# Kernel tuning notes

Measured on AMD Instinct MI355X. Metric: run time of the kernel, lower is better.

Reference implementation:

```python
import jax, jax.numpy as jnp
import numpy as np


def decode_e4m3(bits):
    """Decode raw FP8 E4M3 byte patterns (int32 in [0,256)) to float32.

    Layout: 1 sign bit, 4 exponent bits (bias 7), 3 mantissa bits.
    exp==0 -> subnormal: mant/8 * 2^-6. The NaN pattern (exp==15, man==7)
    is remapped to the max normal magnitude 448 to keep the reference
    NaN-free for randomized inputs.
    """
    b = bits.astype(jnp.int32)
    sign = jnp.where((b & 0x80) != 0, -1.0, 1.0).astype(jnp.float32)
    exp = (b >> 3) & 0xF
    man = (b & 0x7).astype(jnp.float32)
    # remap NaN encoding (exp=15, man=7) to max normal 448 = (1+6/8)*2^8
    man = jnp.where((exp == 15) & (man == 7.0), 6.0, man)
    sub = man * jnp.float32(2.0 ** -9)                     # man/8 * 2^-6
    norm = (1.0 + man / 8.0) * jnp.exp2((exp - 7).astype(jnp.float32))
    return sign * jnp.where(exp == 0, sub, norm)


def setup_inputs() -> dict:
    key = jax.random.key(0)
    k1, k2, k3, k4 = jax.random.split(key, 4)
    T, D_IN, D_OUT = 8192, 4096, 8192  # tokens (2x4096), in_features, out_features
    x = jax.random.normal(k1, (T, D_IN), dtype=jnp.float32)
    weight_fp8 = jax.random.randint(k2, (D_OUT, D_IN), 0, 256, dtype=jnp.int32)
    weight_scales = jax.random.uniform(k3, (D_OUT,), dtype=jnp.float32)
    bias = jax.random.normal(k4, (D_OUT,), dtype=jnp.float32)
    return {"x": x, "weight_fp8": weight_fp8, "weight_scales": weight_scales, "bias": bias}


def reference(x, weight_fp8, weight_scales, bias):
    # Fused FP8 dequant + GEMM + bias: W = decode(w_fp8) * scale[:, None]
    w = decode_e4m3(weight_fp8) * weight_scales[:, None]   # [out, in]
    return jnp.einsum("ti,oi->to", x, w) + bias[None, :]
```

## Files before the change

### kernel.cpp

```cpp
#include <hip/hip_runtime.h>

using short8 = __attribute__((ext_vector_type(8))) short;
using bf16x8 = __attribute__((ext_vector_type(8))) __bf16;
using f32x4  = __attribute__((ext_vector_type(4))) float;

__device__ __forceinline__ void gload_lds16(const void* g, void* l) {
  __builtin_amdgcn_global_load_lds(
      (const __attribute__((address_space(1))) void*)g,
      (__attribute__((address_space(3))) void*)l, 16, 0, 0);
}


__device__ __forceinline__ float dec_e4m3(int b) {
  int e = (b >> 3) & 15;
  int m = b & 7;
  if (e == 15 && m == 7) m = 6;
  float v;
  if (e) v = (1.0f + (float)m * 0.125f) * __uint_as_float((unsigned)(e + 120) << 23);
  else   v = (float)m * 0.001953125f;
  return (b & 0x80) ? -v : v;
}

__global__ void dec_w_kernel(const int* __restrict__ wq,
                             unsigned short* __restrict__ wb, int n8) {
  int i = blockIdx.x * blockDim.x + threadIdx.x;
  if (i >= n8) return;
  const int4* p = (const int4*)wq + (size_t)i * 2;
  int4 a = p[0], b4 = p[1];
  int bv[8] = {a.x, a.y, a.z, a.w, b4.x, b4.y, b4.z, b4.w};
  short8 r;
#pragma unroll
  for (int j = 0; j < 8; ++j) {
    float f = dec_e4m3(bv[j]);
    r[j] = (short)(__float_as_uint(f) >> 16);
  }
  *(short8*)(wb + (size_t)i * 8) = r;
}

__global__ void cvt_x_kernel(const float* __restrict__ x,
                             unsigned short* __restrict__ xb, int n8) {
  int i = blockIdx.x * blockDim.x + threadIdx.x;
  if (i >= n8) return;
  const float4* p = (const float4*)x + (size_t)i * 2;
  float4 a = p[0], b4 = p[1];
  float v[8] = {a.x, a.y, a.z, a.w, b4.x, b4.y, b4.z, b4.w};
  short8 r;
#pragma unroll
  for (int j = 0; j < 8; ++j) {
    unsigned u = __float_as_uint(v[j]);
    u += 0x7FFFu + ((u >> 16) & 1u);
    r[j] = (short)(u >> 16);
  }
  *(short8*)(xb + (size_t)i * 8) = r;
}


#define NOPV ((void)0)
#define VM6 asm volatile("s_waitcnt vmcnt(6)" ::: "memory")
#define VM0 asm volatile("s_waitcnt vmcnt(0)" ::: "memory")

#define STAGE_A(GP, LBUF, KT, J) do { \
    const char* _g = (GP) + (size_t)(KT) * 128u; \
    gload_lds16(_g + (size_t)((J) * 64) * Kb, (LBUF) + ((J) * 64) * 128 + tdA); \
    gload_lds16(_g + (size_t)(128 + (J) * 64) * Kb, (LBUF) + (128 + (J) * 64) * 128 + tdA); \
  } while (0)

#define STAGE_B(GP, LBUF, KT, J) do { \
    const char* _g = (GP) + (size_t)(KT) * 128u; \
    gload_lds16(_g + (size_t)((J) * 32) * Kb, (LBUF) + ((J) * 32) * 128 + tdB); \
    gload_lds16(_g + (size_t)(128 + (J) * 32) * Kb, (LBUF) + (128 + (J) * 32) * 128 + tdB); \
  } while (0)

#define PHASE(QM, QN, DOA, DOB, STAGE, LGK8, VM) { \
    if (DOA) { \
      _Pragma("unroll") \
      for (int mi = 0; mi < 4; ++mi) { \
        const char* _b = lA + (size_t)(arow + (QM) * 64 + mi * 16) * 128; \
        a[mi][0] = *(const bf16x8*)(_b + fo0); \
        a[mi][1] = *(const bf16x8*)(_b + fo1); \
      } \
    } \
    if (DOB) { \
      _Pragma("unroll") \
      for (int ni = 0; ni < 2; ++ni) { \
        const char* _b = lB + (size_t)(brow + ((QN) * 2 + ni) * 16) * 128; \
        b[(QN) * 2 + ni][0] = *(const bf16x8*)(_b + fo0); \
        b[(QN) * 2 + ni][1] = *(const bf16x8*)(_b + fo1); \
      } \
    } \
    STAGE; \
    if (LGK8) asm volatile("s_waitcnt lgkmcnt(8)" ::: "memory"); \
    __builtin_amdgcn_s_barrier(); \
    asm volatile("s_waitcnt lgkmcnt(0)" ::: "memory"); \
    __builtin_amdgcn_sched_barrier(0); \
    __builtin_amdgcn_s_setprio(1); \
    _Pragma("unroll") \
    for (int mi = 0; mi < 4; ++mi) \
      _Pragma("unroll") \
      for (int ni = 0; ni < 2; ++ni) \
        _Pragma("unroll") \
        for (int ks = 0; ks < 2; ++ks) \
          acc[(QM) * 4 + mi][(QN) * 2 + ni] = __builtin_amdgcn_mfma_f32_16x16x32_bf16( \
              a[mi][ks], b[(QN) * 2 + ni][ks], acc[(QM) * 4 + mi][(QN) * 2 + ni], 0, 0, 0); \
    __builtin_amdgcn_s_setprio(0); \
    VM; \
    __builtin_amdgcn_s_barrier(); \
  }

__global__ __launch_bounds__(512, 2) void gemm256_kernel(
    const unsigned short* __restrict__ A, const unsigned short* __restrict__ B,
    const float* __restrict__ scale, const float* __restrict__ bias,
    float* __restrict__ out, int T, int K, int N) {
  extern __shared__ char lds[];
  char* const lA0 = lds;
  char* const lB0 = lds + 32768;
  char* const lA1 = lds + 65536;
  char* const lB1 = lds + 98304;

  const int nbn = N >> 8;
  const int nbm = T >> 8;
  int bm, bn, CH;
  if (((nbm & 3) == 0) && ((nbn & 7) == 0) &&
      (int)gridDim.x == (nbm >> 2) * nbn) {
    const int xcd = blockIdx.x & 7, off = blockIdx.x >> 3;
    const int cpx = nbn >> 3;
    const int col = xcd * cpx + (off % cpx);
    const int ci  = off / cpx;
    bm = (ci * 4) << 8;
    bn = col << 8;
    CH = 4;
  } else {
    const int nwg = nbm * nbn;
    const int q = nwg >> 3, r = nwg & 7;
    const int xcd = blockIdx.x & 7, off = blockIdx.x >> 3;
    const int swz = (xcd < r ? xcd * (q + 1) : r * (q + 1) + (xcd - r) * q) + off;
    bm = (swz / nbn) << 8;
    bn = (swz % nbn) << 8;
    CH = 1;
  }

  const int tid = threadIdx.x;
  const int wave = tid >> 6, lane = tid & 63;
  const int wm = wave >> 2, wn = wave & 3;
  const int nt = K >> 6;
  const size_t Kb = (size_t)K * 2;

  const int trow = tid >> 3;
  const int gcol = ((tid & 7) * 16) ^ (((tid >> 3) & 7) << 4);
  const int bmap = ((tid & 256) ? 64 : 0) + ((tid >> 6) & 3) * 8 + ((tid >> 3) & 7);
  const char* gAb = (const char*)A + (size_t)(bm + trow) * Kb + gcol;
  const char* gBb = (const char*)B + (size_t)(bn + bmap) * Kb + gcol;
  const int tdA = tid * 16;
  const int tdB = bmap * 128 + (tid & 7) * 16;

  const int g16 = lane >> 4, l8 = lane & 7;
  const int fo0 = ((g16 ^ l8) << 4);
  const int fo1 = fo0 ^ 64;
  const int arow = wm * 128 + (lane & 15);
  const int brow = wn * 64 + (lane & 15);

  const int ccol = bn + wn * 64 + (lane & 15);
  int crow = bm + wm * 128 + ((lane >> 4) << 2);
  float scv[4], biv[4];
#pragma unroll
  for (int ni = 0; ni < 4; ++ni) {
    scv[ni] = scale[ccol + ni * 16];
    biv[ni] = bias[ccol + ni * 16];
  }

  f32x4 acc[8][4] = {};
  bf16x8 a[4][2], b[4][2];
  const char *lA, *lB;

  for (int ch = 0; ch < CH; ++ch) {
    const bool more = (ch + 1 < CH);
    const char* gAn = gAb + (size_t)256 * Kb;

    if (ch == 0) {
      STAGE_A(gAb, lA0, 0, 0);
      STAGE_B(gBb, lB0, 0, 0);
      STAGE_B(gBb, lB0, 0, 1);
      STAGE_A(gAb, lA0, 0, 1);
      STAGE_A(gAb, lA1, 1, 0);
      STAGE_B(gBb, lB1, 1, 0);
      STAGE_B(gBb, lB1, 1, 1);
      VM6;
      __builtin_amdgcn_s_barrier();
    }

    int t = 0;
    for (; t + 3 < nt; t += 2) {
      lA = lA0; lB = lB0;
      PHASE(0, 0, 1, 1, STAGE_A(gAb, lA1, t + 1, 1), 1, NOPV)
      PHASE(0, 1, 0, 1, STAGE_A(gAb, lA0, t + 2, 0), 0, NOPV)
      PHASE(1, 1, 1, 0, STAGE_B(gBb, lB0, t + 2, 0), 0, NOPV)
      PHASE(1, 0, 0, 0, STAGE_B(gBb, lB0, t + 2, 1), 0, VM6)
      lA = lA1; lB = lB1;
      PHASE(0, 0, 1, 1, STAGE_A(gAb, lA0, t + 2, 1), 1, NOPV)
      PHASE(0, 1, 0, 1, STAGE_A(gAb, lA1, t + 3, 0), 0, NOPV)
      PHASE(1, 1, 1, 0, STAGE_B(gBb, lB1, t + 3, 0), 0, NOPV)
      PHASE(1, 0, 0, 0, STAGE_B(gBb, lB1, t + 3, 1), 0, VM6)
    }
    lA = lA0; lB = lB0;
    PHASE(0, 0, 1, 1, STAGE_A(gAb, lA1, t + 1, 1), 1, NOPV)
    PHASE(0, 1, 0, 1, NOPV, 0, NOPV)
    PHASE(1, 1, 1, 0, NOPV, 0, NOPV)
    PHASE(1, 0, 0, 0, NOPV, 0, VM0)
    lA = lA1; lB = lB1;
    PHASE(0, 0, 1, 1, { if (more) STAGE_A(gAn, lA0, 0, 0); }, 1, NOPV)
    PHASE(0, 1, 0, 1, { if (more) STAGE_B(gBb, lB0, 0, 0); }, 0, NOPV)
    PHASE(1, 1, 1, 0, { if (more) STAGE_B(gBb, lB0, 0, 1); }, 0, NOPV)
    PHASE(1, 0, 0, 0, { if (more) STAGE_A(gAn, lA0, 0, 1); }, 0, NOPV)

#pragma unroll
    for (int ni = 0; ni < 4; ++ni) {
      const int o = ccol + ni * 16;
#pragma unroll
      for (int mi = 0; mi < 8; ++mi) {
#pragma unroll
        for (int rr = 0; rr < 4; ++rr) {
          __builtin_nontemporal_store(acc[mi][ni][rr] * scv[ni] + biv[ni],
                                      &out[(size_t)(crow + mi * 16 + rr) * N + o]);
        }
      }
    }

    if (more) {
#pragma unroll
      for (int mi = 0; mi < 8; ++mi)
#pragma unroll
        for (int ni = 0; ni < 4; ++ni)
          acc[mi][ni] = (f32x4){0.f, 0.f, 0.f, 0.f};
      STAGE_A(gAn, lA1, 1, 0);
      STAGE_B(gBb, lB1, 1, 0);
      STAGE_B(gBb, lB1, 1, 1);
      VM6;
      __builtin_amdgcn_s_barrier();
      gAb = gAn;
      crow += 256;
    }
  }
}


#define BM 128
#define BN 128
#define BK 64

__global__ __launch_bounds__(256) void gemm_bf16_kernel(
    const unsigned short* __restrict__ A, const unsigned short* __restrict__ B,
    const float* __restrict__ scale, const float* __restrict__ bias,
    float* __restrict__ out, int T, int K, int N) {
  __shared__ __align__(16) unsigned short lsA[BM * BK];
  __shared__ __align__(16) unsigned short lsB[BN * BK];

  const int nbn = N / BN;
  const int nwg = (T / BM) * nbn;
  const int q = nwg >> 3, r = nwg & 7;
  const int xcd = blockIdx.x & 7, off = blockIdx.x >> 3;
  const int swz = (xcd < r ? xcd * (q + 1) : r * (q + 1) + (xcd - r) * q) + off;
  const int bm = (swz / nbn) * BM;
  const int bn = (swz % nbn) * BN;

  const int tid = threadIdx.x;
  const int wave = tid >> 6, lane = tid & 63;
  const int wm = (wave >> 1) * 64, wn = (wave & 1) * 64;

  f32x4 acc[4][4] = {};

  const int srow = (wave << 3) + (lane >> 3);
  const int scolb = (lane & 7) * 16;
  const size_t Kb = (size_t)K * 2;
  const char* gA = (const char*)A + (size_t)bm * Kb + scolb;
  const char* gB = (const char*)B + (size_t)bn * Kb + scolb;
  char* laddrA = (char*)lsA + wave * 1024;
  char* laddrB = (char*)lsB + wave * 1024;

  for (int k0 = 0; k0 < K; k0 += BK) {
    const char* pa = gA + (size_t)k0 * 2;
    const char* pb = gB + (size_t)k0 * 2;
#pragma unroll
    for (int s = 0; s < 4; ++s) {
      int row = s * 32 + srow;
      gload_lds16(pa + (size_t)row * Kb, laddrA + s * 4096);
      gload_lds16(pb + (size_t)row * Kb, laddrB + s * 4096);
    }
    __syncthreads();

    const int arow2 = wm + (lane & 15);
    const int brow2 = wn + (lane & 15);
#pragma unroll
    for (int kk = 0; kk < BK; kk += 32) {
      const int kcol = kk + ((lane >> 4) << 3);
      bf16x8 af[4], bfr[4];
#pragma unroll
      for (int i = 0; i < 4; ++i)
        af[i] = *(const bf16x8*)(lsA + (size_t)(arow2 + i * 16) * BK + kcol);
#pragma unroll
      for (int i = 0; i < 4; ++i)
        bfr[i] = *(const bf16x8*)(lsB + (size_t)(brow2 + i * 16) * BK + kcol);
#pragma unroll
      for (int mi = 0; mi < 4; ++mi)
#pragma unroll
        for (int ni = 0; ni < 4; ++ni)
          acc[mi][ni] = __builtin_amdgcn_mfma_f32_16x16x32_bf16(
              af[mi], bfr[ni], acc[mi][ni], 0, 0, 0);
    }
    __syncthreads();
  }

  const int ccol = bn + wn + (lane & 15);
  const int crow0 = bm + wm + ((lane >> 4) << 2);
#pragma unroll
  for (int ni = 0; ni < 4; ++ni) {
    const int o = ccol + ni * 16;
    const float sc = scale[o], bi = bias[o];
#pragma unroll
    for (int mi = 0; mi < 4; ++mi) {
#pragma unroll
      for (int rr = 0; rr < 4; ++rr) {
        const int t2 = crow0 + mi * 16 + rr;
        out[(size_t)t2 * N + o] = acc[mi][ni][rr] * sc + bi;
      }
    }
  }
}


__global__ void naive_kernel(const float* __restrict__ X, const int* __restrict__ Wq,
                             const float* __restrict__ sc, const float* __restrict__ bs,
                             float* __restrict__ out, int T, int K, int N) {
  __shared__ float xt[16][16];
  __shared__ float wt[16][17];
  const int tx = threadIdx.x & 15, ty = threadIdx.x >> 4;
  const int t = blockIdx.y * 16 + ty, o = blockIdx.x * 16 + tx;
  float acc = 0.f;
  for (int k0 = 0; k0 < K; k0 += 16) {
    xt[ty][tx] = X[(size_t)t * K + k0 + tx];
    wt[ty][tx] = dec_e4m3(Wq[(size_t)(blockIdx.x * 16 + ty) * K + k0 + tx]);
    __syncthreads();
#pragma unroll
    for (int kk = 0; kk < 16; ++kk) acc += xt[ty][kk] * wt[tx][kk];
    __syncthreads();
  }
  out[(size_t)t * N + o] = acc * sc[o] + bs[o];
}

extern "C" void kernel_launch(void* const* d_in, const int* in_sizes, int n_in,
                              void* d_out, int out_size, void* d_ws, size_t ws_size,
                              hipStream_t stream) {
  const float* x  = (const float*)d_in[0];
  const int*   wq = (const int*)d_in[1];
  const float* sc = (const float*)d_in[2];
  const float* bi = (const float*)d_in[3];
  float* out = (float*)d_out;

  const int DOUT = in_sizes[2];
  const int DIN  = in_sizes[1] / DOUT;
  const int T    = in_sizes[0] / DIN;

  const size_t need = ((size_t)T * DIN + (size_t)DOUT * DIN) * 2;
  const bool ok256 = (T % 256 == 0) && (DOUT % 256 == 0) && (DIN % 256 == 0);
  const bool ok128 = (T % BM == 0) && (DOUT % BN == 0) && (DIN % BK == 0);

  if (ws_size >= need && (ok256 || ok128)) {
    unsigned short* xb = (unsigned short*)d_ws;
    unsigned short* wb = xb + (size_t)T * DIN;
    const int nx8 = (int)((size_t)T * DIN / 8);
    const int nw8 = (int)((size_t)DOUT * DIN / 8);
    cvt_x_kernel<<<(nx8 + 255) / 256, 256, 0, stream>>>(x, xb, nx8);
    dec_w_kernel<<<(nw8 + 255) / 256, 256, 0, stream>>>(wq, wb, nw8);
    if (ok256) {
      const int nbm = T >> 8, nbn = DOUT >> 8;
      const bool okchain = ((nbm & 3) == 0) && ((nbn & 7) == 0);
      const int grid = okchain ? (nbm >> 2) * nbn : nbm * nbn;
      gemm256_kernel<<<grid, 512, 131072, stream>>>(xb, wb, sc, bi, out, T, DIN, DOUT);
    } else {
      dim3 grid((T / BM) * (DOUT / BN));
      gemm_bf16_kernel<<<grid, 256, 0, stream>>>(xb, wb, sc, bi, out, T, DIN, DOUT);
    }
  } else {
    dim3 g(DOUT / 16, T / 16);
    naive_kernel<<<g, 256, 0, stream>>>(x, wq, sc, bi, out, T, DIN, DOUT);
  }
}
```

Baseline: 515.2 us.

## Software-pipeline LDS fragment reads one phase ahead of MFMA compute

```diff
diff --git a/kernel.cpp b/kernel.cpp
--- a/kernel.cpp
+++ b/kernel.cpp
@@ -71,26 +71,25 @@
     gload_lds16(_g + (size_t)(128 + (J) * 32) * Kb, (LBUF) + (128 + (J) * 32) * 128 + tdB); \
   } while (0)
 
-#define PHASE(QM, QN, DOA, DOB, STAGE, LGK8, VM) { \
-    if (DOA) { \
-      _Pragma("unroll") \
-      for (int mi = 0; mi < 4; ++mi) { \
-        const char* _b = lA + (size_t)(arow + (QM) * 64 + mi * 16) * 128; \
-        a[mi][0] = *(const bf16x8*)(_b + fo0); \
-        a[mi][1] = *(const bf16x8*)(_b + fo1); \
-      } \
+#define RD_A(DST, LB, QM) do { \
+    _Pragma("unroll") \
+    for (int mi = 0; mi < 4; ++mi) { \
+      const char* _b = lds + (LB) + (size_t)(arow + (QM) * 64 + mi * 16) * 128; \
+      (DST)[mi * 2 + 0] = *(const bf16x8*)(_b + fo0); \
+      (DST)[mi * 2 + 1] = *(const bf16x8*)(_b + fo1); \
     } \
-    if (DOB) { \
-      _Pragma("unroll") \
-      for (int ni = 0; ni < 2; ++ni) { \
-        const char* _b = lB + (size_t)(brow + ((QN) * 2 + ni) * 16) * 128; \
-        b[(QN) * 2 + ni][0] = *(const bf16x8*)(_b + fo0); \
-        b[(QN) * 2 + ni][1] = *(const bf16x8*)(_b + fo1); \
-      } \
+  } while (0)
+
+#define RD_B(DST, LB, QN) do { \
+    _Pragma("unroll") \
+    for (int ni = 0; ni < 2; ++ni) { \
+      const char* _b = lds + (LB) + (size_t)(brow + ((QN) * 2 + ni) * 16) * 128; \
+      (DST)[ni * 2 + 0] = *(const bf16x8*)(_b + fo0); \
+      (DST)[ni * 2 + 1] = *(const bf16x8*)(_b + fo1); \
     } \
-    STAGE; \
-    if (LGK8) asm volatile("s_waitcnt lgkmcnt(8)" ::: "memory"); \
-    __builtin_amdgcn_s_barrier(); \
+  } while (0)
+
+#define PH(AB, BB, QM, QN, STBLK, VMBLK, PFBLK) do { \
     asm volatile("s_waitcnt lgkmcnt(0)" ::: "memory"); \
     __builtin_amdgcn_sched_barrier(0); \
     __builtin_amdgcn_s_setprio(1); \
@@ -101,11 +100,13 @@
         _Pragma("unroll") \
         for (int ks = 0; ks < 2; ++ks) \
           acc[(QM) * 4 + mi][(QN) * 2 + ni] = __builtin_amdgcn_mfma_f32_16x16x32_bf16( \
-              a[mi][ks], b[(QN) * 2 + ni][ks], acc[(QM) * 4 + mi][(QN) * 2 + ni], 0, 0, 0); \
+              (AB)[mi * 2 + ks], (BB)[ni * 2 + ks], acc[(QM) * 4 + mi][(QN) * 2 + ni], 0, 0, 0); \
     __builtin_amdgcn_s_setprio(0); \
-    VM; \
+    STBLK; \
+    VMBLK; \
+    PFBLK; \
     __builtin_amdgcn_s_barrier(); \
-  }
+  } while (0)
 
 __global__ __launch_bounds__(512, 2) void gemm256_kernel(
     const unsigned short* __restrict__ A, const unsigned short* __restrict__ B,
@@ -116,6 +117,7 @@
   char* const lB0 = lds + 32768;
   char* const lA1 = lds + 65536;
   char* const lB1 = lds + 98304;
+  const int L0A = 0, L0B = 32768, L1A = 65536, L1B = 98304;
 
   const int nbn = N >> 8;
   const int nbm = T >> 8;
@@ -169,8 +171,7 @@
   }
 
   f32x4 acc[8][4] = {};
-  bf16x8 a[4][2], b[4][2];
-  const char *lA, *lB;
+  bf16x8 aE[8], aO[8], b0a[4], b0b[4], b1[4];
 
   for (int ch = 0; ch < CH; ++ch) {
     const bool more = (ch + 1 < CH);
@@ -186,31 +187,31 @@
       STAGE_B(gBb, lB1, 1, 1);
       VM6;
       __builtin_amdgcn_s_barrier();
+      RD_A(aE, L0A, 0);
+      RD_B(b0a, L0B, 0);
     }
 
     int t = 0;
     for (; t + 3 < nt; t += 2) {
-      lA = lA0; lB = lB0;
-      PHASE(0, 0, 1, 1, STAGE_A(gAb, lA1, t + 1, 1), 1, NOPV)
-      PHASE(0, 1, 0, 1, STAGE_A(gAb, lA0, t + 2, 0), 0, NOPV)
-      PHASE(1, 1, 1, 0, STAGE_B(gBb, lB0, t + 2, 0), 0, NOPV)
-      PHASE(1, 0, 0, 0, STAGE_B(gBb, lB0, t + 2, 1), 0, VM6)
-      lA = lA1; lB = lB1;
-      PHASE(0, 0, 1, 1, STAGE_A(gAb, lA0, t + 2, 1), 1, NOPV)
-      PHASE(0, 1, 0, 1, STAGE_A(gAb, lA1, t + 3, 0), 0, NOPV)
-      PHASE(1, 1, 1, 0, STAGE_B(gBb, lB1, t + 3, 0), 0, NOPV)
-      PHASE(1, 0, 0, 0, STAGE_B(gBb, lB1, t + 3, 1), 0, VM6)
-    }
-    lA = lA0; lB = lB0;
-    PHASE(0, 0, 1, 1, STAGE_A(gAb, lA1, t + 1, 1), 1, NOPV)
-    PHASE(0, 1, 0, 1, NOPV, 0, NOPV)
-    PHASE(1, 1, 1, 0, NOPV, 0, NOPV)
-    PHASE(1, 0, 0, 0, NOPV, 0, VM0)
-    lA = lA1; lB = lB1;
-    PHASE(0, 0, 1, 1, { if (more) STAGE_A(gAn, lA0, 0, 0); }, 1, NOPV)
-    PHASE(0, 1, 0, 1, { if (more) STAGE_B(gBb, lB0, 0, 0); }, 0, NOPV)
-    PHASE(1, 1, 1, 0, { if (more) STAGE_B(gBb, lB0, 0, 1); }, 0, NOPV)
-    PHASE(1, 0, 0, 0, { if (more) STAGE_A(gAn, lA0, 0, 1); }, 0, NOPV)
+      PH(aE, b0a, 0, 0, STAGE_A(gAb, lA1, t + 1, 1), NOPV, RD_B(b1, L0B, 1));
+      PH(aE, b1,  0, 1, STAGE_A(gAb, lA0, t + 2, 0), NOPV, RD_A(aO, L0A, 1));
+      PH(aO, b1,  1, 1, STAGE_B(gBb, lB0, t + 2, 0), NOPV, NOPV);
+      PH(aO, b0a, 1, 0, STAGE_B(gBb, lB0, t + 2, 1), VM6,
+         { RD_A(aE, L1A, 0); RD_B(b0b, L1B, 0); });
+      PH(aE, b0b, 0, 0, STAGE_A(gAb, lA0, t + 2, 1), NOPV, RD_B(b1, L1B, 1));
+      PH(aE, b1,  0, 1, STAGE_A(gAb, lA1, t + 3, 0), NOPV, RD_A(aO, L1A, 1));
+      PH(aO, b1,  1, 1, STAGE_B(gBb, lB1, t + 3, 0), NOPV, NOPV);
+      PH(aO, b0b, 1, 0, STAGE_B(gBb, lB1, t + 3, 1), VM6,
+         { RD_A(aE, L0A, 0); RD_B(b0a, L0B, 0); });
+    }
+    PH(aE, b0a, 0, 0, STAGE_A(gAb, lA1, t + 1, 1), NOPV, RD_B(b1, L0B, 1));
+    PH(aE, b1,  0, 1, NOPV, NOPV, RD_A(aO, L0A, 1));
+    PH(aO, b1,  1, 1, NOPV, NOPV, NOPV);
+    PH(aO, b0a, 1, 0, NOPV, VM0, { RD_A(aE, L1A, 0); RD_B(b0b, L1B, 0); });
+    PH(aE, b0b, 0, 0, { if (more) STAGE_A(gAn, lA0, 0, 0); }, NOPV, RD_B(b1, L1B, 1));
+    PH(aE, b1,  0, 1, { if (more) STAGE_B(gBb, lB0, 0, 0); }, NOPV, RD_A(aO, L1A, 1));
+    PH(aO, b1,  1, 1, { if (more) STAGE_B(gBb, lB0, 0, 1); }, NOPV, NOPV);
+    PH(aO, b0b, 1, 0, { if (more) STAGE_A(gAn, lA0, 0, 1); }, NOPV, NOPV);
 
 #pragma unroll
     for (int ni = 0; ni < 4; ++ni) {
@@ -236,6 +237,8 @@
       STAGE_B(gBb, lB1, 1, 1);
       VM6;
       __builtin_amdgcn_s_barrier();
+      RD_A(aE, L0A, 0);
+      RD_B(b0a, L0B, 0);
       gAb = gAn;
       crow += 256;
     }
```

Result: no change. 517.1 us (+0.4%).
